# Kernel optimization log

Hardware: AMD Instinct MI355X
Metric: run time of the kernel (lower is better)

The kernel has to match this reference:

```python
import jax, jax.numpy as jnp
import numpy as np
from jax import lax

CONF_THRES = 0.25
IOU_THRES = 0.45
MAX_DET = 300      # detections kept after NMS
TOPK = 1024        # candidates entering NMS (sorted by score)
MAX_WH = 7680.0    # class offset for class-aware NMS
NC = 80            # classes
NM = 32            # mask prototypes
IMG = 640          # network input size
PROTO_HW = 160     # proto map resolution (IMG/4)
EPS = 1e-7


def xywh2xyxy(x):
    cx, cy, w, h = x[:, 0], x[:, 1], x[:, 2], x[:, 3]
    return jnp.stack([cx - w / 2, cy - h / 2, cx + w / 2, cy + h / 2], axis=1)


def box_iou(box1, box2):
    # box1: [K,4], box2: [M,4] in xyxy -> [K,M]
    a1, a2 = box1[:, None, :2], box1[:, None, 2:]
    b1, b2 = box2[None, :, :2], box2[None, :, 2:]
    inter = jnp.clip(jnp.minimum(a2, b2) - jnp.maximum(a1, b1), 0).prod(-1)
    area1 = (a2 - a1).prod(-1)
    area2 = (b2 - b1).prod(-1)
    return inter / (area1 + area2 - inter + EPS)


def greedy_nms_keep(boxes, valid, iou_thres):
    # boxes already sorted by descending score; returns bool keep mask [K]
    K = boxes.shape[0]
    sup = box_iou(boxes, boxes) > iou_thres  # [K,K]
    lower = jnp.arange(K)

    def body(i, keep):
        suppressed = jnp.any(keep & sup[:, i] & (lower < i))
        return keep.at[i].set(valid[i] & ~suppressed)

    return lax.fori_loop(0, K, body, jnp.zeros((K,), dtype=bool))


def setup_inputs() -> dict:
    key = jax.random.key(0)
    k1, k2, k3, k4, k5, k6 = jax.random.split(key, 6)
    N = 25200
    cxcy = jax.random.uniform(k1, (1, N, 2), jnp.float32, 0.0, float(IMG))
    wh = jax.random.uniform(k2, (1, N, 2), jnp.float32, 5.0, 120.0)
    obj = jax.random.uniform(k3, (1, N, 1), jnp.float32)
    cls = jax.random.uniform(k4, (1, N, NC), jnp.float32)
    coef = jax.random.normal(k5, (1, N, NM), jnp.float32) * 0.5
    prediction = jnp.concatenate([cxcy, wh, obj, cls, coef], axis=2)  # [1,N,117]
    protos = jax.random.normal(k6, (NM, PROTO_HW, PROTO_HW), jnp.float32)
    return {"prediction": prediction, "protos": protos}


def reference(prediction, protos):
    x = prediction[0]                       # [N, 5+NC+NM]
    obj = x[:, 4]
    cls_conf = x[:, 5:5 + NC] * obj[:, None]  # x[:,5:] *= x[:,4:5]
    conf = cls_conf.max(axis=1)
    j = jnp.argmax(cls_conf, axis=1)
    valid_all = (obj > CONF_THRES) & (conf > CONF_THRES)

    boxes_all = xywh2xyxy(x[:, :4])
    scores_masked = jnp.where(valid_all, conf, -1.0)
    top_scores, idx = lax.top_k(scores_masked, TOPK)  # sorted descending

    b = boxes_all[idx]              # [TOPK,4], no class offset
    cls_id = j[idx]                 # [TOPK]
    coef = x[idx, 5 + NC:]          # [TOPK,NM]
    valid = top_scores > CONF_THRES

    nms_boxes = b + (cls_id.astype(b.dtype) * MAX_WH)[:, None]  # class-aware
    keep = greedy_nms_keep(nms_boxes, valid, IOU_THRES)

    keep_scores = jnp.where(keep, top_scores, -1.0)
    fs, i2 = lax.top_k(keep_scores, MAX_DET)
    fvalid = fs > CONF_THRES
    fb = b[i2] * fvalid[:, None].astype(b.dtype)
    fcls = jnp.where(fvalid, cls_id[i2], -1)
    fcoef = coef[i2] * fvalid[:, None].astype(coef.dtype)
    fs = jnp.where(fvalid, fs, 0.0)

    # process_mask_native
    m = jax.nn.sigmoid(fcoef @ protos.reshape(NM, -1))          # [MAX_DET, HW*HW]
    m = m.reshape(MAX_DET, PROTO_HW, PROTO_HW)
    m = jax.image.resize(m, (MAX_DET, IMG, IMG), method='bilinear')
    x1, y1, x2, y2 = fb[:, 0], fb[:, 1], fb[:, 2], fb[:, 3]
    r = jnp.arange(IMG, dtype=fb.dtype)[None, None, :]  # along width vs x
    c = jnp.arange(IMG, dtype=fb.dtype)[None, :, None]  # along height vs y
    crop = ((r >= x1[:, None, None]) & (r < x2[:, None, None]) &
            (c >= y1[:, None, None]) & (c < y2[:, None, None]))
    masks_f = m * crop.astype(m.dtype) * fvalid[:, None, None].astype(m.dtype)
    masks_bool = masks_f > 0.5
    return masks_f, masks_bool, fb, fs, fcls
```

## Files before the change

### kernel.cpp

```cpp
#include <hip/hip_runtime.h>

constexpr int   kNA     = 25200;
constexpr int   kStride = 117;
constexpr int   kNC     = 80;
constexpr int   kNM     = 32;
constexpr int   kTopK   = 1024;
constexpr int   kMaxDet = 300;
constexpr int   kImg    = 640;
constexpr int   kPHW    = 160;
constexpr float kConfT  = 0.25f;
constexpr float kIouT   = 0.45f;
constexpr float kMaxWH  = 7680.0f;

constexpr unsigned long long kMaskElems = 300ull * 640ull * 640ull;

typedef float v4f __attribute__((ext_vector_type(4)));

constexpr size_t O_SCORES = 0;
constexpr size_t O_BOXES  = 100864;
constexpr size_t O_CLS    = 504064;
constexpr size_t O_TKIDX  = 604864;
constexpr size_t O_TKSC   = 608960;
constexpr size_t O_TKBOX  = 613056;
constexpr size_t O_TKNBOX = 629440;
constexpr size_t O_TKCLS  = 645824;
constexpr size_t O_SUP    = 649984;
constexpr size_t O_NDET   = 782336;
constexpr size_t O_DBOX   = 782400;
constexpr size_t O_DCOEF  = 787264;

__global__ __launch_bounds__(256) void zero_k(float* __restrict__ out) {
    const size_t n4 = (2ull * kMaskElems) >> 2;
    const size_t stride = (size_t)gridDim.x * 256;
    v4f z = 0.f;
    for (size_t i = (size_t)blockIdx.x * 256 + threadIdx.x; i < n4; i += stride)
        __builtin_nontemporal_store(z, ((v4f*)out) + i);
}

constexpr int kDecRows = 64;
constexpr int kDecThr  = 128;
__global__ __launch_bounds__(kDecThr) void decode_k(const float* __restrict__ pred,
        float* __restrict__ scores, float* __restrict__ boxes, int* __restrict__ cls) {
    __shared__ float rows[kDecRows * kStride];
    int base = blockIdx.x * kDecRows;
    int nrows = min(kDecRows, kNA - base);
    int total = nrows * kStride;
    const float* src = pred + (size_t)base * kStride;
    for (int i = threadIdx.x; i < total; i += kDecThr) rows[i] = src[i];
    __syncthreads();
    int r = threadIdx.x;
    if (r >= nrows) return;
    int a = base + r;
    const float* p = rows + r * kStride;
    float obj = p[4];
    float best = -1.0f; int bj = 0;
    for (int c = 0; c < kNC; ++c) {
        float v = p[5 + c] * obj;
        if (v > best) { best = v; bj = c; }
    }
    bool valid = (obj > kConfT) && (best > kConfT);
    scores[a] = valid ? best : -1.0f;
    float cx = p[0], cy = p[1], w = p[2], h = p[3];
    float hw = w * 0.5f, hh = h * 0.5f;
    boxes[4*a+0] = cx - hw; boxes[4*a+1] = cy - hh;
    boxes[4*a+2] = cx + hw; boxes[4*a+3] = cy + hh;
    cls[a] = bj;
}

__device__ __forceinline__ unsigned f2ord(float f) {
    unsigned b = __float_as_uint(f);
    return (b & 0x80000000u) ? ~b : (b | 0x80000000u);
}
__device__ __forceinline__ float ord2f(unsigned u) {
    unsigned b = (u & 0x80000000u) ? (u ^ 0x80000000u) : ~u;
    return __uint_as_float(b);
}

__global__ __launch_bounds__(1024) void topk_k(const float* __restrict__ scores,
        const float* __restrict__ boxes, const int* __restrict__ cls,
        int* __restrict__ tk_idx, float* __restrict__ tk_sc, float* __restrict__ tk_box,
        float* __restrict__ tk_nbox, int* __restrict__ tk_cls) {
    __shared__ unsigned long long keys[kTopK];
    __shared__ int wcnt[16];
    __shared__ unsigned sh_cnt;
    int tid = threadIdx.x;
    int lane = tid & 63, wid = tid >> 6;

    unsigned uv[25];
#pragma unroll
    for (int k = 0; k < 25; ++k) {
        int i = tid + k * 1024;
        uv[k] = (i < kNA) ? f2ord(scores[i]) : 0u;
    }

    unsigned lo = 0, hi = 0xFFFFFFFFu;
    for (int it = 0; it < 32; ++it) {
        unsigned mid = (unsigned)(((unsigned long long)lo + (unsigned long long)hi) >> 1);
        if (mid == lo) break;
        int c = 0;
#pragma unroll
        for (int k = 0; k < 25; ++k) c += (uv[k] >= mid);
#pragma unroll
        for (int off = 32; off >= 1; off >>= 1) c += __shfl_down(c, off);
        __syncthreads();
        if (lane == 0) wcnt[wid] = c;
        __syncthreads();
        int tot = 0;
#pragma unroll
        for (int w = 0; w < 16; ++w) tot += wcnt[w];
        if (tot >= kTopK) lo = mid; else hi = mid;
    }
    unsigned uT = lo;

    int nGreater;
    {
        int c = 0;
#pragma unroll
        for (int k = 0; k < 25; ++k) c += (uv[k] >= uT + 1u);
#pragma unroll
        for (int off = 32; off >= 1; off >>= 1) c += __shfl_down(c, off);
        __syncthreads();
        if (lane == 0) wcnt[wid] = c;
        __syncthreads();
        int t = 0;
#pragma unroll
        for (int w = 0; w < 16; ++w) t += wcnt[w];
        nGreater = t;
    }
    int krem = kTopK - nGreater;
    if (tid == 0) sh_cnt = 0;
    __syncthreads();

#pragma unroll
    for (int k = 0; k < 25; ++k) {
        int i = tid + k * 1024;
        unsigned u = uv[k];
        if (i < kNA && u > uT) {
            unsigned p = atomicAdd(&sh_cnt, 1u);
            keys[p] = ((unsigned long long)u << 32) | (unsigned)(~i);
        }
    }

    int ilo = 0, ihi = kNA;
    while (ilo < ihi) {
        int mid = (ilo + ihi) >> 1;
        int c = 0;
#pragma unroll
        for (int k = 0; k < 25; ++k) {
            int i = tid + k * 1024;
            c += (i < mid && uv[k] == uT);
        }
#pragma unroll
        for (int off = 32; off >= 1; off >>= 1) c += __shfl_down(c, off);
        __syncthreads();
        if (lane == 0) wcnt[wid] = c;
        __syncthreads();
        int cc = 0;
#pragma unroll
        for (int w = 0; w < 16; ++w) cc += wcnt[w];
        if (cc >= krem) ihi = mid; else ilo = mid + 1;
    }
#pragma unroll
    for (int k = 0; k < 25; ++k) {
        int i = tid + k * 1024;
        if (i < ilo && uv[k] == uT) {
            unsigned p = atomicAdd(&sh_cnt, 1u);
            keys[p] = ((unsigned long long)uT << 32) | (unsigned)(~i);
        }
    }
    __syncthreads();

    for (int k2 = 2; k2 <= kTopK; k2 <<= 1) {
        for (int j = k2 >> 1; j > 0; j >>= 1) {
            int partner = tid ^ j;
            unsigned long long a = keys[tid], b = keys[partner];
            bool iLower = (tid & j) == 0;
            bool descRegion = (tid & k2) == 0;
            unsigned long long mx = (a > b) ? a : b;
            unsigned long long mn = (a > b) ? b : a;
            unsigned long long res = (iLower == descRegion) ? mx : mn;
            __syncthreads();
            keys[tid] = res;
            __syncthreads();
        }
    }

    unsigned long long key = keys[tid];
    unsigned u = (unsigned)(key >> 32);
    int idx = (int)(~((unsigned)key));
    tk_idx[tid] = idx;
    tk_sc[tid]  = ord2f(u);
    float4 bx = ((const float4*)boxes)[idx];
    ((float4*)tk_box)[tid] = bx;
    int cid = cls[idx];
    float off = (float)cid * kMaxWH;
    float4 nb; nb.x = bx.x + off; nb.y = bx.y + off; nb.z = bx.z + off; nb.w = bx.w + off;
    ((float4*)tk_nbox)[tid] = nb;
    tk_cls[tid] = cid;
}

__global__ __launch_bounds__(256) void supmat_k(const float* __restrict__ tk_nbox,
                                                unsigned long long* __restrict__ sup) {
    __shared__ float4 bxs[kTopK];
    int tid = threadIdx.x;
    for (int k = tid; k < kTopK; k += 256) bxs[k] = ((const float4*)tk_nbox)[k];
    __syncthreads();
    int r = tid >> 4, w = tid & 15;
    int i = blockIdx.x * 16 + r;
    float4 a = bxs[i];
    float areaA = (a.z - a.x) * (a.w - a.y);
    unsigned long long bits = 0;
    for (int l = 0; l < 64; ++l) {
        float4 b = bxs[w * 64 + l];
        float xx1 = fmaxf(a.x, b.x), yy1 = fmaxf(a.y, b.y);
        float xx2 = fminf(a.z, b.z), yy2 = fminf(a.w, b.w);
        float iw = fmaxf(xx2 - xx1, 0.f), ih = fmaxf(yy2 - yy1, 0.f);
        float inter = iw * ih;
        float areaB = (b.z - b.x) * (b.w - b.y);
        float iou = inter / (areaA + areaB - inter + 1e-7f);
        if (iou > kIouT) bits |= 1ull << l;
    }
    sup[(size_t)i * 16 + w] = bits;
}

__global__ __launch_bounds__(256) void nms_k(const float* __restrict__ pred,
        const float* __restrict__ tk_sc, const int* __restrict__ tk_idx,
        const float* __restrict__ tk_box, const int* __restrict__ tk_cls,
        const unsigned long long* __restrict__ sup,
        int* __restrict__ ndet, float* __restrict__ out,
        float* __restrict__ dbox, float* __restrict__ dcoef) {
    __shared__ unsigned long long buf[2][1024];
    __shared__ int dslot_lds[kMaxDet];
    __shared__ int sh_nd;
    int tid = threadIdx.x;
    int lane = tid & 63;

    unsigned long long vW = 0;
    if (tid < 64) {
        for (int b = 0; b < 16; ++b) {
            unsigned long long bw = __ballot(tk_sc[b * 64 + lane] > kConfT);
            if (lane == b) vW = bw;
        }
    }
    for (int i = tid; i < 1024; i += 256) buf[0][i] = sup[i];

    unsigned long long supW = 0;
    unsigned long long kws[16];
    for (int b = 0; b < 16; ++b) {
        __syncthreads();
        if (tid >= 64) {
            if (b + 1 < 16) {
                for (int i = tid - 64; i < 1024; i += 192)
                    buf[(b + 1) & 1][i] = sup[(size_t)(b + 1) * 1024 + i];
            }
        } else {
            const unsigned long long* ch = buf[b & 1];
            unsigned long long s  = __shfl(supW, b);
            unsigned long long vb = __shfl(vW, b);
            unsigned long long kw = 0;
            unsigned long long rbuf[8];
            int w16 = lane & 15;
#pragma unroll
            for (int p = 0; p < 8; ++p) rbuf[p] = ch[p * 16 + w16];
            for (int l = 0; l < 64; ++l) {
                unsigned long long rw = rbuf[l & 7];
                if (l + 8 < 64) rbuf[l & 7] = ch[(l + 8) * 16 + w16];
                unsigned long long rb = __shfl(rw, b);
                bool kp = ((vb >> l) & 1ull) && !((s >> l) & 1ull);
                if (kp) { kw |= 1ull << l; s |= rb; supW |= rw; }
            }
            kws[b] = kw;
        }
    }
    if (tid == 0) {
        int d = 0;
        for (int b = 0; b < 16 && d < kMaxDet; ++b) {
            unsigned long long kw = kws[b];
            for (int l = 0; l < 64 && d < kMaxDet; ++l)
                if ((kw >> l) & 1ull) dslot_lds[d++] = b * 64 + l;
        }
        sh_nd = d;
        *ndet = d;
    }
    __syncthreads();

    int n = sh_nd;
    float* fb   = out + 2 * kMaskElems;
    float* fs   = fb + kMaxDet * 4;
    float* fcls = fs + kMaxDet;
    for (int d = tid; d < kMaxDet; d += 256) {
        if (d < n) {
            int t = dslot_lds[d];
            int a = tk_idx[t];
            float4 bx = ((const float4*)tk_box)[t];
            fb[4*d+0] = bx.x; fb[4*d+1] = bx.y; fb[4*d+2] = bx.z; fb[4*d+3] = bx.w;
            fs[d] = tk_sc[t];
            fcls[d] = (float)tk_cls[t];
            ((float4*)dbox)[d] = bx;
            const float* cp = pred + (size_t)a * kStride + 5 + kNC;
            for (int c = 0; c < kNM; ++c) dcoef[d * kNM + c] = cp[c];
        } else {
            fb[4*d+0] = 0.f; fb[4*d+1] = 0.f; fb[4*d+2] = 0.f; fb[4*d+3] = 0.f;
            fs[d] = 0.f; fcls[d] = -1.0f;
            float4 z; z.x = z.y = z.z = z.w = 0.f;
            ((float4*)dbox)[d] = z;
            for (int c = 0; c < kNM; ++c) dcoef[d * kNM + c] = 0.f;
        }
    }
}

constexpr int kPatch = 34;

__global__ __launch_bounds__(256) void patch_k(const float* __restrict__ protos,
        const float* __restrict__ dbox, const float* __restrict__ dcoef,
        const int* __restrict__ ndet, float* __restrict__ out) {
    int d = blockIdx.x;
    if (d >= *ndet) return;
    float4 bx = ((const float4*)dbox)[d];
    float x1 = bx.x, y1 = bx.y, x2 = bx.z, y2 = bx.w;

    int i_lo = max(0, (int)ceilf(y1));
    int i_hi = min(kImg - 1, (int)ceilf(y2) - 1);
    int j_lo = max(0, (int)ceilf(x1));
    int j_hi = min(kImg - 1, (int)ceilf(x2) - 1);
    if (i_lo > i_hi || j_lo > j_hi) return;

    int py_lo = min(159, max(0, (int)floorf(((float)i_lo + 0.5f) * 0.25f - 0.5f)));
    int py_hi = min(159, max(0, (int)floorf(((float)i_hi + 0.5f) * 0.25f - 0.5f) + 1));
    int px_lo = min(159, max(0, (int)floorf(((float)j_lo + 0.5f) * 0.25f - 0.5f)));
    int px_hi = min(159, max(0, (int)floorf(((float)j_hi + 0.5f) * 0.25f - 0.5f) + 1));
    int ph = py_hi - py_lo + 1, pw = px_hi - px_lo + 1;
    if (ph > kPatch) ph = kPatch;
    if (pw > kPatch) pw = kPatch;

    int tid = threadIdx.x;
    __shared__ float coef[kNM];
    __shared__ float patch[kPatch * kPatch];
    if (tid < kNM) coef[tid] = dcoef[d * kNM + tid];
    __syncthreads();
    int cells = ph * pw;
    for (int c = tid; c < cells; c += 256) {
        int py = py_lo + c / pw, px = px_lo + c % pw;
        const float* pp = protos + (size_t)py * kPHW + px;
        float z = 0.f;
#pragma unroll
        for (int m = 0; m < kNM; ++m) z = fmaf(coef[m], pp[(size_t)m * kPHW * kPHW], z);
        patch[c] = 1.0f / (1.0f + expf(-z));
    }
    __syncthreads();

    float* mf = out + (size_t)d * (kImg * kImg);
    float* mb = out + kMaskElems + (size_t)d * (kImg * kImg);
    int W = j_hi - j_lo + 1;
    int H = i_hi - i_lo + 1;
    int dr = tid >> 7, dc = tid & 127;
    for (int rr = dr; rr < H; rr += 2) {
        int i = i_lo + rr;
        float sy = fminf(fmaxf(((float)i + 0.5f) * 0.25f - 0.5f, 0.f), 159.f);
        int yy0 = (int)sy; float fy = sy - (float)yy0;
        int yy1i = min(yy0 + 1, 159);
        const float* prow0 = &patch[(yy0 - py_lo) * pw - px_lo];
        const float* prow1 = &patch[(yy1i - py_lo) * pw - px_lo];
        for (int cc = dc; cc < W; cc += 128) {
            int j = j_lo + cc;
            float sx = fminf(fmaxf(((float)j + 0.5f) * 0.25f - 0.5f, 0.f), 159.f);
            int xx0 = (int)sx; float fx = sx - (float)xx0;
            int xx1i = min(xx0 + 1, 159);
            float v00 = prow0[xx0], v01 = prow0[xx1i];
            float v10 = prow1[xx0], v11 = prow1[xx1i];
            float top = (1.f - fx) * v00 + fx * v01;
            float bot = (1.f - fx) * v10 + fx * v11;
            float m = (1.f - fy) * top + fy * bot;
            mf[(size_t)i * kImg + j] = m;
            mb[(size_t)i * kImg + j] = (m > 0.5f) ? 1.f : 0.f;
        }
    }
}

extern "C" void kernel_launch(void* const* d_in, const int* in_sizes, int n_in,
                              void* d_out, int out_size, void* d_ws, size_t ws_size,
                              hipStream_t stream) {
    const float* pred   = (const float*)d_in[0];
    const float* protos = (const float*)d_in[1];
    float* out = (float*)d_out;
    char* ws = (char*)d_ws;

    float* s_scores = (float*)(ws + O_SCORES);
    float* s_boxes  = (float*)(ws + O_BOXES);
    int*   s_cls    = (int*)  (ws + O_CLS);
    int*   tk_idx   = (int*)  (ws + O_TKIDX);
    float* tk_sc    = (float*)(ws + O_TKSC);
    float* tk_box   = (float*)(ws + O_TKBOX);
    float* tk_nbox  = (float*)(ws + O_TKNBOX);
    int*   tk_cls   = (int*)  (ws + O_TKCLS);
    unsigned long long* sup = (unsigned long long*)(ws + O_SUP);
    int*   ndet     = (int*)  (ws + O_NDET);
    float* dbox     = (float*)(ws + O_DBOX);
    float* dcoef    = (float*)(ws + O_DCOEF);

    zero_k<<<dim3(2048), dim3(256), 0, stream>>>(out);
    decode_k<<<dim3((kNA + kDecRows - 1) / kDecRows), dim3(kDecThr), 0, stream>>>(pred, s_scores, s_boxes, s_cls);
    topk_k<<<dim3(1), dim3(1024), 0, stream>>>(s_scores, s_boxes, s_cls,
                                               tk_idx, tk_sc, tk_box, tk_nbox, tk_cls);
    supmat_k<<<dim3(64), dim3(256), 0, stream>>>(tk_nbox, sup);
    nms_k<<<dim3(1), dim3(256), 0, stream>>>(pred, tk_sc, tk_idx, tk_box, tk_cls, sup,
                                             ndet, out, dbox, dcoef);
    patch_k<<<dim3(kMaxDet), dim3(256), 0, stream>>>(protos, dbox, dcoef, ndet, out);
}
```

Measured before the change: 1.289 ms.

## Overlap output zeroing with serial top-k, suppression and NMS kernels

```diff
diff --git a/kernel.cpp b/kernel.cpp
--- a/kernel.cpp
+++ b/kernel.cpp
@@ -15,6 +15,14 @@
 constexpr unsigned long long kMaskElems = 300ull * 640ull * 640ull;
 
 typedef float v4f __attribute__((ext_vector_type(4)));
+
+constexpr size_t kN4     = (2ull * kMaskElems) >> 2;
+constexpr size_t kZA_end = 27648000;
+constexpr size_t kZB_end = 33792000;
+
+constexpr int kZTopk = 512;
+constexpr int kZSup  = 256;
+constexpr int kZNms  = 1024;
 
 constexpr size_t O_SCORES = 0;
 constexpr size_t O_BOXES  = 100864;
@@ -29,14 +37,6 @@
 constexpr size_t O_DBOX   = 782400;
 constexpr size_t O_DCOEF  = 787264;
 
-__global__ __launch_bounds__(256) void zero_k(float* __restrict__ out) {
-    const size_t n4 = (2ull * kMaskElems) >> 2;
-    const size_t stride = (size_t)gridDim.x * 256;
-    v4f z = 0.f;
-    for (size_t i = (size_t)blockIdx.x * 256 + threadIdx.x; i < n4; i += stride)
-        __builtin_nontemporal_store(z, ((v4f*)out) + i);
-}
-
 constexpr int kDecRows = 64;
 constexpr int kDecThr  = 128;
 __global__ __launch_bounds__(kDecThr) void decode_k(const float* __restrict__ pred,
@@ -79,7 +79,15 @@
 __global__ __launch_bounds__(1024) void topk_k(const float* __restrict__ scores,
         const float* __restrict__ boxes, const int* __restrict__ cls,
         int* __restrict__ tk_idx, float* __restrict__ tk_sc, float* __restrict__ tk_box,
-        float* __restrict__ tk_nbox, int* __restrict__ tk_cls) {
+        float* __restrict__ tk_nbox, int* __restrict__ tk_cls,
+        float* __restrict__ outz) {
+    if (blockIdx.x != 0) {
+        v4f z = 0.f;
+        size_t stride = (size_t)(gridDim.x - 1) * 1024;
+        for (size_t i = (size_t)(blockIdx.x - 1) * 1024 + threadIdx.x; i < kZA_end; i += stride)
+            __builtin_nontemporal_store(z, ((v4f*)outz) + i);
+        return;
+    }
     __shared__ unsigned long long keys[kTopK];
     __shared__ int wcnt[16];
     __shared__ unsigned sh_cnt;
@@ -93,10 +101,16 @@
         uv[k] = (i < kNA) ? f2ord(scores[i]) : 0u;
     }
 
-    unsigned lo = 0, hi = 0xFFFFFFFFu;
-    for (int it = 0; it < 32; ++it) {
-        unsigned mid = (unsigned)(((unsigned long long)lo + (unsigned long long)hi) >> 1);
-        if (mid == lo) break;
+    unsigned lo = 0u, hi = 0xFFFFFFFFu;
+    for (int it = 0; it < 34; ++it) {
+        unsigned mid;
+        if (it == 0)      mid = 0xBE800000u;
+        else if (it == 1) mid = 0xBF800001u;
+        else {
+            mid = (unsigned)(((unsigned long long)lo + (unsigned long long)hi) >> 1);
+            if (mid == lo) break;
+        }
+        if (mid <= lo || mid >= hi) continue;
         int c = 0;
 #pragma unroll
         for (int k = 0; k < 25; ++k) c += (uv[k] >= mid);
@@ -200,7 +214,16 @@
 }
 
 __global__ __launch_bounds__(256) void supmat_k(const float* __restrict__ tk_nbox,
-                                                unsigned long long* __restrict__ sup) {
+                                                unsigned long long* __restrict__ sup,
+                                                float* __restrict__ outz) {
+    if (blockIdx.x >= 64) {
+        v4f z = 0.f;
+        size_t stride = (size_t)(gridDim.x - 64) * 256;
+        for (size_t i = kZA_end + (size_t)(blockIdx.x - 64) * 256 + threadIdx.x;
+             i < kZB_end; i += stride)
+            __builtin_nontemporal_store(z, ((v4f*)outz) + i);
+        return;
+    }
     __shared__ float4 bxs[kTopK];
     int tid = threadIdx.x;
     for (int k = tid; k < kTopK; k += 256) bxs[k] = ((const float4*)tk_nbox)[k];
@@ -229,6 +252,14 @@
         const unsigned long long* __restrict__ sup,
         int* __restrict__ ndet, float* __restrict__ out,
         float* __restrict__ dbox, float* __restrict__ dcoef) {
+    if (blockIdx.x != 0) {
+        v4f z = 0.f;
+        size_t stride = (size_t)(gridDim.x - 1) * 256;
+        for (size_t i = kZB_end + (size_t)(blockIdx.x - 1) * 256 + threadIdx.x;
+             i < kN4; i += stride)
+            __builtin_nontemporal_store(z, ((v4f*)out) + i);
+        return;
+    }
     __shared__ unsigned long long buf[2][1024];
     __shared__ int dslot_lds[kMaxDet];
     __shared__ int sh_nd;
@@ -398,12 +429,11 @@
     float* dbox     = (float*)(ws + O_DBOX);
     float* dcoef    = (float*)(ws + O_DCOEF);
 
-    zero_k<<<dim3(2048), dim3(256), 0, stream>>>(out);
     decode_k<<<dim3((kNA + kDecRows - 1) / kDecRows), dim3(kDecThr), 0, stream>>>(pred, s_scores, s_boxes, s_cls);
-    topk_k<<<dim3(1), dim3(1024), 0, stream>>>(s_scores, s_boxes, s_cls,
-                                               tk_idx, tk_sc, tk_box, tk_nbox, tk_cls);
-    supmat_k<<<dim3(64), dim3(256), 0, stream>>>(tk_nbox, sup);
-    nms_k<<<dim3(1), dim3(256), 0, stream>>>(pred, tk_sc, tk_idx, tk_box, tk_cls, sup,
+    topk_k<<<dim3(1 + kZTopk), dim3(1024), 0, stream>>>(s_scores, s_boxes, s_cls,
+                                               tk_idx, tk_sc, tk_box, tk_nbox, tk_cls, out);
+    supmat_k<<<dim3(64 + kZSup), dim3(256), 0, stream>>>(tk_nbox, sup, out);
+    nms_k<<<dim3(1 + kZNms), dim3(256), 0, stream>>>(pred, tk_sc, tk_idx, tk_box, tk_cls, sup,
                                              ndet, out, dbox, dcoef);
     patch_k<<<dim3(kMaxDet), dim3(256), 0, stream>>>(protos, dbox, dcoef, ndet, out);
 }
```

Result: faster. 1.113 ms (-13.6%).
